# Performance work log

Measured on AMD Instinct MI355X. Metric: run time of the kernel, lower is better.

The kernel has to match this reference:

```python
import jax, jax.numpy as jnp
import numpy as np


def _quantize(mat):
    # per-row (last-dim) symmetric int8 quantization; scale stored in fp16 like torch
    max_val = (jnp.max(jnp.abs(mat), axis=-1) / 127.0).astype(jnp.float16)
    # torch's .to(int8) truncates toward zero; jnp astype does the same for in-range values
    q = (mat / max_val[..., None].astype(mat.dtype)).astype(jnp.int8)
    return q, max_val


def setup_inputs() -> dict:
    key = jax.random.key(0)
    k1, k2, k3, k4 = jax.random.split(key, 4)
    B, S, D_IN, D_OUT = 4, 2048, 4096, 4096
    x = jax.random.normal(k1, (B, S, D_IN), dtype=jnp.float32)
    origin_weight = jax.random.normal(k2, (D_OUT, D_IN), dtype=jnp.float32) * 0.02
    bias = jax.random.normal(k3, (D_OUT,), dtype=jnp.float32) * 0.01
    act_max = jax.random.normal(k4, (D_IN,), dtype=jnp.float32)
    return {"x": x, "origin_weight": origin_weight, "bias": bias,
            "act_max": act_max, "alpha": 32}


def reference(x, origin_weight, bias, act_max, alpha):
    d_in = act_max.shape[-1]
    # get_unq_idx_topk: top-alpha outlier channels by |act_max|
    _, idx = jax.lax.top_k(jnp.abs(act_max), alpha)          # [alpha]
    t = jnp.ones((d_in,), dtype=origin_weight.dtype).at[idx].set(0)

    # weight decomposition + quantization (done in __init__ in torch)
    weight_q, w_max = _quantize(origin_weight * t)           # [out,in] int8, [out] fp16
    weight_unq = origin_weight[:, idx].T                      # [alpha, out]

    # activation decomposition + per-token quantization
    x_unq = x[..., idx]                                       # [B,S,alpha]
    x_q, x_max = _quantize(x * t.astype(x.dtype))             # [B,S,in] int8, [B,S] fp16

    # simulated MatMulInteger: int8 values multiplied in fp32
    res_q = jnp.matmul(x_q.astype(jnp.float32), weight_q.T.astype(jnp.float32))  # [B,S,out]
    mx = (x_max[..., None] * w_max[None, :]).astype(jnp.float32)                  # [B,S,out]
    res_q = (res_q * mx).astype(x.dtype)

    # fp outlier path
    res_unq = jnp.matmul(x_unq, weight_unq) + bias
    return res_q + res_unq
```

## Files before the change

kernel.cpp:

```cpp
#include <hip/hip_runtime.h>
#include <hip/hip_fp16.h>

typedef __attribute__((ext_vector_type(4)))  int   i32x4;
typedef __attribute__((ext_vector_type(16))) int   i32x16;

#define ALPHA 32
#define BM 256
#define BN 128
#define BK 64


__global__ __launch_bounds__(256) void topk_kernel(const float* __restrict__ act_max,
                                                   int* __restrict__ idx_out,
                                                   unsigned* __restrict__ tbits,
                                                   int K) {
  __shared__ float v[4096];
  __shared__ float rv[4];
  __shared__ int   ri[4];
  __shared__ unsigned bits[128];
  const int t = threadIdx.x;
  for (int i = t; i < K; i += 256) v[i] = fabsf(act_max[i]);
  for (int i = t; i < K / 32; i += 256) bits[i] = 0xFFFFFFFFu;
  __syncthreads();
  for (int sel = 0; sel < ALPHA; ++sel) {
    float bv = -1.f; int bi = 0;
    for (int i = t; i < K; i += 256) {
      float x = v[i];
      if (x > bv) { bv = x; bi = i; }
    }
    for (int m = 1; m < 64; m <<= 1) {
      float ov = __shfl_xor(bv, m);
      int   oi = __shfl_xor(bi, m);
      if (ov > bv || (ov == bv && oi < bi)) { bv = ov; bi = oi; }
    }
    if ((t & 63) == 0) { rv[t >> 6] = bv; ri[t >> 6] = bi; }
    __syncthreads();
    if (t == 0) {
      for (int u = 1; u < 4; ++u)
        if (rv[u] > bv || (rv[u] == bv && ri[u] < bi)) { bv = rv[u]; bi = ri[u]; }
      idx_out[sel] = bi;
      v[bi] = -2.f;
      bits[bi >> 5] &= ~(1u << (bi & 31));
    }
    __syncthreads();
  }
  for (int i = t; i < K / 32; i += 256) tbits[i] = bits[i];
}

__global__ __launch_bounds__(256) void quant8_kernel(
    const float* __restrict__ srcW, const float* __restrict__ srcX,
    const unsigned* __restrict__ tbits, const int* __restrict__ idxg,
    signed char* __restrict__ wq, signed char* __restrict__ xq,
    _Float16* __restrict__ wmax, _Float16* __restrict__ xmax,
    float* __restrict__ wuf, float* __restrict__ xuf,
    int nbw, int K, int N, int M) {
  const int t = threadIdx.x, lane = t & 63, w = t >> 6;
  const int b = blockIdx.x;
  const float* src; signed char* q; _Float16* smax; float* unq; int r0, R;
  if (b < nbw) { src = srcW; q = wq; smax = wmax; unq = wuf; r0 = b * 8; R = N; }
  else         { src = srcX; q = xq; smax = xmax; unq = xuf; r0 = (b - nbw) * 8; R = M; }
  __shared__ unsigned bits[128];
  __shared__ signed char qt[8 * 4096];
  for (int i = t; i < 128; i += 256) bits[i] = tbits[i];
  __syncthreads();
  const int shft = (lane & 7) * 4;
#pragma unroll
  for (int g = 0; g < 2; ++g) {
    const int rl = w + 4 * g;
    const float4* srow = (const float4*)(src + (size_t)(r0 + rl) * K);
    float4 v[16];
    float am = 0.f;
#pragma unroll
    for (int j = 0; j < 16; ++j) {
      float4 x = srow[j * 64 + lane];
      unsigned b4 = bits[j * 8 + (lane >> 3)] >> shft;
      if (!(b4 & 1u)) x.x = 0.f;
      if (!(b4 & 2u)) x.y = 0.f;
      if (!(b4 & 4u)) x.z = 0.f;
      if (!(b4 & 8u)) x.w = 0.f;
      v[j] = x;
      am = fmaxf(am, fmaxf(fmaxf(fabsf(x.x), fabsf(x.y)), fmaxf(fabsf(x.z), fabsf(x.w))));
    }
#pragma unroll
    for (int m = 1; m < 64; m <<= 1) am = fmaxf(am, __shfl_xor(am, m));
    const _Float16 sh = (_Float16)(am / 127.0f);
    const float s = (float)sh;
    if (lane == 0) smax[r0 + rl] = sh;
    signed char* row = qt + rl * 4096;
#pragma unroll
    for (int j = 0; j < 16; ++j) {
      float4 x = v[j];
      char4 c;
      c.x = (signed char)(x.x / s);
      c.y = (signed char)(x.y / s);
      c.z = (signed char)(x.z / s);
      c.w = (signed char)(x.w / s);
      const int c2 = j * 16 + (lane >> 2);
      *(char4*)(row + ((c2 ^ rl) << 4) + (lane & 3) * 4) = c;
    }
  }
  __syncthreads();
  const size_t pbase = (size_t)(r0 >> 5) * 32 * K + (size_t)(r0 & 31) * 16;
#pragma unroll
  for (int i = 0; i < 8; ++i) {
    const int s2 = i * 256 + t;
    const int c2 = s2 >> 3, rl = s2 & 7;
    int4 d = *(const int4*)(qt + rl * 4096 + ((c2 ^ rl) << 4));
    *(int4*)(q + pbase + (size_t)c2 * 512 + rl * 16) = d;
  }
  {
    const int j = t >> 3, rl = t & 7;
    unq[(size_t)j * R + r0 + rl] = src[(size_t)(r0 + rl) * K + idxg[j]];
  }
}

__device__ __forceinline__ void gld_lds16(const signed char* g, signed char* l) {
  __builtin_amdgcn_global_load_lds(
      (const __attribute__((address_space(1))) void*)g,
      (__attribute__((address_space(3))) void*)l, 16, 0, 0);
}

__global__ __launch_bounds__(256, 2) void gemm_kernel(
    const signed char* __restrict__ xq, const signed char* __restrict__ wq,
    const _Float16* __restrict__ xmax, const _Float16* __restrict__ wmax,
    const float* __restrict__ xuf,
    const float* __restrict__ wuf,
    const float* __restrict__ bias,
    float* __restrict__ out, int M, int N, int K) {
  __shared__ union {
    signed char A[4][BM * BK];
    struct { float xu[ALPHA * BM]; float wu[ALPHA * BN]; } e;
  } sm;
  __shared__ _Float16 xmh[BM];
  __shared__ _Float16 wmh[BN];
  __shared__ float    bl[BN];

  const int t = threadIdx.x;
  const int bid = blockIdx.y * gridDim.x + blockIdx.x;
  const int xcd = bid & 7, loc = bid >> 3;
  const int bxi = xcd * 4 + (loc & 3);
  const int byi = loc >> 2;
  const int bm0 = byi * BM;
  const int bn0 = bxi * BN;
  const int lane = t & 63, w = t >> 6;
  const int wm = w >> 1, wn = w & 1;
  const int hi = lane >> 5, l31 = lane & 31;

  i32x16 acc[4][2] = {};

  const size_t P32 = (size_t)32 * K;
  const signed char* aS = xq + (size_t)bm0 * K + (size_t)(t >> 7) * P32 + (t & 127) * 16;
  signed char* const aD = &sm.A[0][0] + t * 16;
  const signed char* bW = wq + (size_t)(bn0 + wn * 64) * K + hi * 512 + l31 * 16;

#define STAGE_A(BUF, KT)                                                          \
  {                                                                               \
    const size_t ko = (size_t)(KT) * 2048;                                        \
    _Pragma("unroll") for (int i = 0; i < 4; ++i)                                 \
      gld_lds16(aS + (size_t)(2 * i) * P32 + ko, aD + (BUF) * (BM * BK) + i * 4096); \
  }

#define LOADB(DST, KT)                                                            \
  _Pragma("unroll") for (int ni = 0; ni < 2; ++ni)                                \
    _Pragma("unroll") for (int ks = 0; ks < 2; ++ks)                              \
      DST[ni][ks] = *(const i32x4*)(bW + (size_t)ni * 32 * K +                    \
                                    (size_t)(KT) * 2048 + ks * 1024);

#define ITER(KT, BCUR, BNXT, WCNT, DOB, DOST)                                     \
  {                                                                               \
    asm volatile("s_waitcnt vmcnt(" #WCNT ")" ::: "memory");                      \
    asm volatile("s_barrier" ::: "memory");                                       \
    if (DOB) { LOADB(BNXT, (KT) + 1); }                                           \
    if (DOST) { STAGE_A(((KT) + 2) & 3, (KT) + 2); }                              \
    const signed char* aRd = &sm.A[(KT) & 3][0] + (wm * 4) * 2048 + hi * 512 + l31 * 16; \
    i32x4 af[2][4];                                                               \
    _Pragma("unroll") for (int ks = 0; ks < 2; ++ks)                              \
      _Pragma("unroll") for (int mi = 0; mi < 4; ++mi)                            \
        af[ks][mi] = *(const i32x4*)(aRd + mi * 2048 + ks * 1024);                \
    __builtin_amdgcn_s_setprio(1);                                                \
    _Pragma("unroll") for (int ks = 0; ks < 2; ++ks)                              \
      _Pragma("unroll") for (int ni = 0; ni < 2; ++ni)                            \
        _Pragma("unroll") for (int mi = 0; mi < 4; ++mi)                          \
          acc[mi][ni] = __builtin_amdgcn_mfma_i32_32x32x32_i8(                    \
              af[ks][mi], BCUR[ni][ks], acc[mi][ni], 0, 0, 0);                    \
    __builtin_amdgcn_s_setprio(0);                                                \
  }

  const int NT = K >> 6;
  i32x4 bA[2][2], bB[2][2];
  STAGE_A(0, 0);
  STAGE_A(1, 1);
  LOADB(bA, 0);

  int kt = 0;
  for (; kt < NT - 2; kt += 2) {
    ITER(kt,     bA, bB, 8, true, true);
    ITER(kt + 1, bB, bA, 8, true, (kt + 3 < NT));
  }
  ITER(NT - 2, bA, bB, 8, true,  false);
  ITER(NT - 1, bB, bA, 4, false, false);
#undef ITER
#undef LOADB
#undef STAGE_A

  __syncthreads();
  {
    const float4* xs = (const float4*)xuf;
    float4* xl = (float4*)sm.e.xu;
#pragma unroll
    for (int i = 0; i < 8; ++i) {
      int p = i * 256 + t;
      int j = p >> 6, r4 = p & 63;
      xl[p] = xs[(size_t)j * (M >> 2) + (bm0 >> 2) + r4];
    }
    const float4* wsrc = (const float4*)wuf;
    float4* wl = (float4*)sm.e.wu;
#pragma unroll
    for (int i = 0; i < 4; ++i) {
      int p = i * 256 + t;
      int j = p >> 5, r4 = p & 31;
      wl[p] = wsrc[(size_t)j * (N >> 2) + (bn0 >> 2) + r4];
    }
    if (t < BM / 2) ((unsigned*)xmh)[t] = ((const unsigned*)(xmax + bm0))[t];
    if (t < BN / 2) ((unsigned*)wmh)[t] = ((const unsigned*)(wmax + bn0))[t];
    if (t < BN / 4) ((float4*)bl)[t] = ((const float4*)(bias + bn0))[t];
  }
  __syncthreads();

  const int c0 = wn * 64 + l31;
  const _Float16 wh0 = wmh[c0], wh1 = wmh[c0 + 32];
  const float bv0 = bl[c0], bv1 = bl[c0 + 32];
  const float* xul = sm.e.xu;
  const float* wul = sm.e.wu;

#pragma unroll
  for (int mi = 0; mi < 4; ++mi) {
    const int rbase = wm * 128 + mi * 32 + 4 * hi;
    float f0[16], f1[16];
#pragma unroll
    for (int r = 0; r < 16; ++r) {
      int row = rbase + (r & 3) + 8 * (r >> 2);
      _Float16 xh = xmh[row];
      float mx0 = (float)(_Float16)(xh * wh0);
      float mx1 = (float)(_Float16)(xh * wh1);
      f0[r] = (float)acc[mi][0][r] * mx0 + bv0;
      f1[r] = (float)acc[mi][1][r] * mx1 + bv1;
    }
#pragma unroll 4
    for (int j = 0; j < ALPHA; ++j) {
      const float4* xrow4 = (const float4*)(xul + j * BM + rbase);
      float wv0 = wul[j * BN + c0];
      float wv1 = wul[j * BN + c0 + 32];
#pragma unroll
      for (int gq = 0; gq < 4; ++gq) {
        float4 xv = xrow4[gq * 2];
        f0[gq * 4 + 0] += xv.x * wv0;  f1[gq * 4 + 0] += xv.x * wv1;
        f0[gq * 4 + 1] += xv.y * wv0;  f1[gq * 4 + 1] += xv.y * wv1;
        f0[gq * 4 + 2] += xv.z * wv0;  f1[gq * 4 + 2] += xv.z * wv1;
        f0[gq * 4 + 3] += xv.w * wv0;  f1[gq * 4 + 3] += xv.w * wv1;
      }
    }
#pragma unroll
    for (int r = 0; r < 16; ++r) {
      int row = bm0 + rbase + (r & 3) + 8 * (r >> 2);
      size_t o = (size_t)row * N + bn0;
      out[o + c0] = f0[r];
      out[o + c0 + 32] = f1[r];
    }
  }
}

extern "C" void kernel_launch(void* const* d_in, const int* in_sizes, int n_in,
                              void* d_out, int out_size, void* d_ws, size_t ws_size,
                              hipStream_t stream) {
  const float* x       = (const float*)d_in[0];
  const float* W       = (const float*)d_in[1];
  const float* bias    = (const float*)d_in[2];
  const float* act_max = (const float*)d_in[3];
  const int K = in_sizes[3];
  const int N = in_sizes[1] / K;
  const int M = in_sizes[0] / K;
  float* out = (float*)d_out;

  char* ws = (char*)d_ws;
  size_t off = 0;
  auto take = [&](size_t b) { char* p = ws + off; off += (b + 255) & ~(size_t)255; return p; };
  signed char* wq  = (signed char*)take((size_t)N * K);
  signed char* xq  = (signed char*)take((size_t)M * K);
  _Float16* wmax   = (_Float16*)take((size_t)N * 2);
  _Float16* xmax   = (_Float16*)take((size_t)M * 2);
  float* wuf       = (float*)take((size_t)ALPHA * N * 4);
  float* xuf       = (float*)take((size_t)ALPHA * M * 4);
  int* idx         = (int*)take(ALPHA * 4);
  unsigned* tbits  = (unsigned*)take((size_t)(K / 32) * 4);

  const int nbw = N / 8, nbx = M / 8;
  topk_kernel<<<1, 256, 0, stream>>>(act_max, idx, tbits, K);
  quant8_kernel<<<nbw + nbx, 256, 0, stream>>>(W, x, tbits, idx, wq, xq,
                                               wmax, xmax, wuf, xuf, nbw, K, N, M);
  dim3 grid(N / BN, M / BM);
  gemm_kernel<<<grid, 256, 0, stream>>>(xq, wq, xmax, wmax, xuf, wuf, bias, out, M, N, K);
}
```

Before: 288.9 us.

## Load A and B MFMA fragments directly from global into registers, drop LDS staging

Removes the LDS staging of the A tile (global_load_lds with a 4-buffer ring and per-iteration barriers). Each wave now loads both its A and B fragments straight from global memory into registers, using double-buffered register fragments, and no barriers remain in the main loop. This cuts LDS traffic and synchronisation. In exchange, A tiles are no longer shared between the two waves in a row of the block, so global/L2 read traffic for A doubles and register pressure rises.

After: 291.9 us. No clear change (+1.1%).

```diff
diff --git a/kernel.cpp b/kernel.cpp
--- a/kernel.cpp
+++ b/kernel.cpp
@@ -114,11 +114,7 @@
   }
 }
 
-__device__ __forceinline__ void gld_lds16(const signed char* g, signed char* l) {
-  __builtin_amdgcn_global_load_lds(
-      (const __attribute__((address_space(1))) void*)g,
-      (__attribute__((address_space(3))) void*)l, 16, 0, 0);
-}
+typedef struct { i32x4 a[4][2]; i32x4 b[2][2]; } Frag;
 
 __global__ __launch_bounds__(256, 2) void gemm_kernel(
     const signed char* __restrict__ xq, const signed char* __restrict__ wq,
@@ -127,10 +123,7 @@
     const float* __restrict__ wuf,
     const float* __restrict__ bias,
     float* __restrict__ out, int M, int N, int K) {
-  __shared__ union {
-    signed char A[4][BM * BK];
-    struct { float xu[ALPHA * BM]; float wu[ALPHA * BN]; } e;
-  } sm;
+  __shared__ struct { float xu[ALPHA * BM]; float wu[ALPHA * BN]; } sme;
   __shared__ _Float16 xmh[BM];
   __shared__ _Float16 wmh[BN];
   __shared__ float    bl[BN];
@@ -149,64 +142,51 @@
   i32x16 acc[4][2] = {};
 
   const size_t P32 = (size_t)32 * K;
-  const signed char* aS = xq + (size_t)bm0 * K + (size_t)(t >> 7) * P32 + (t & 127) * 16;
-  signed char* const aD = &sm.A[0][0] + t * 16;
-  const signed char* bW = wq + (size_t)(bn0 + wn * 64) * K + hi * 512 + l31 * 16;
-
-#define STAGE_A(BUF, KT)                                                          \
+  const signed char* const aF = xq + ((size_t)(bm0 >> 5) + wm * 4) * P32 + hi * 512 + l31 * 16;
+  const signed char* const bF = wq + ((size_t)(bn0 >> 5) + wn * 2) * P32 + hi * 512 + l31 * 16;
+
+#define LOADT(P, KT)                                                              \
   {                                                                               \
     const size_t ko = (size_t)(KT) * 2048;                                        \
-    _Pragma("unroll") for (int i = 0; i < 4; ++i)                                 \
-      gld_lds16(aS + (size_t)(2 * i) * P32 + ko, aD + (BUF) * (BM * BK) + i * 4096); \
-  }
-
-#define LOADB(DST, KT)                                                            \
-  _Pragma("unroll") for (int ni = 0; ni < 2; ++ni)                                \
-    _Pragma("unroll") for (int ks = 0; ks < 2; ++ks)                              \
-      DST[ni][ks] = *(const i32x4*)(bW + (size_t)ni * 32 * K +                    \
-                                    (size_t)(KT) * 2048 + ks * 1024);
-
-#define ITER(KT, BCUR, BNXT, WCNT, DOB, DOST)                                     \
+    _Pragma("unroll") for (int mi = 0; mi < 4; ++mi)                              \
+      _Pragma("unroll") for (int ks = 0; ks < 2; ++ks)                            \
+        P.a[mi][ks] = *(const i32x4*)(aF + (size_t)mi * P32 + ko + ks * 1024);    \
+    _Pragma("unroll") for (int ni = 0; ni < 2; ++ni)                              \
+      _Pragma("unroll") for (int ks = 0; ks < 2; ++ks)                            \
+        P.b[ni][ks] = *(const i32x4*)(bF + (size_t)ni * P32 + ko + ks * 1024);    \
+  }
+
+#define MFMAT(P)                                                                  \
   {                                                                               \
-    asm volatile("s_waitcnt vmcnt(" #WCNT ")" ::: "memory");                      \
-    asm volatile("s_barrier" ::: "memory");                                       \
-    if (DOB) { LOADB(BNXT, (KT) + 1); }                                           \
-    if (DOST) { STAGE_A(((KT) + 2) & 3, (KT) + 2); }                              \
-    const signed char* aRd = &sm.A[(KT) & 3][0] + (wm * 4) * 2048 + hi * 512 + l31 * 16; \
-    i32x4 af[2][4];                                                               \
+    __builtin_amdgcn_s_setprio(1);                                                \
     _Pragma("unroll") for (int ks = 0; ks < 2; ++ks)                              \
       _Pragma("unroll") for (int mi = 0; mi < 4; ++mi)                            \
-        af[ks][mi] = *(const i32x4*)(aRd + mi * 2048 + ks * 1024);                \
-    __builtin_amdgcn_s_setprio(1);                                                \
-    _Pragma("unroll") for (int ks = 0; ks < 2; ++ks)                              \
-      _Pragma("unroll") for (int ni = 0; ni < 2; ++ni)                            \
-        _Pragma("unroll") for (int mi = 0; mi < 4; ++mi)                          \
+        _Pragma("unroll") for (int ni = 0; ni < 2; ++ni)                          \
           acc[mi][ni] = __builtin_amdgcn_mfma_i32_32x32x32_i8(                    \
-              af[ks][mi], BCUR[ni][ks], acc[mi][ni], 0, 0, 0);                    \
+              P.a[mi][ks], P.b[ni][ks], acc[mi][ni], 0, 0, 0);                    \
     __builtin_amdgcn_s_setprio(0);                                                \
   }
 
   const int NT = K >> 6;
-  i32x4 bA[2][2], bB[2][2];
-  STAGE_A(0, 0);
-  STAGE_A(1, 1);
-  LOADB(bA, 0);
-
+  Frag pA, pB;
+  LOADT(pA, 0);
   int kt = 0;
   for (; kt < NT - 2; kt += 2) {
-    ITER(kt,     bA, bB, 8, true, true);
-    ITER(kt + 1, bB, bA, 8, true, (kt + 3 < NT));
-  }
-  ITER(NT - 2, bA, bB, 8, true,  false);
-  ITER(NT - 1, bB, bA, 4, false, false);
-#undef ITER
-#undef LOADB
-#undef STAGE_A
+    LOADT(pB, kt + 1);
+    MFMAT(pA);
+    LOADT(pA, kt + 2);
+    MFMAT(pB);
+  }
+  LOADT(pB, NT - 1);
+  MFMAT(pA);
+  MFMAT(pB);
+#undef LOADT
+#undef MFMAT
 
   __syncthreads();
   {
     const float4* xs = (const float4*)xuf;
-    float4* xl = (float4*)sm.e.xu;
+    float4* xl = (float4*)sme.xu;
 #pragma unroll
     for (int i = 0; i < 8; ++i) {
       int p = i * 256 + t;
@@ -214,7 +194,7 @@
       xl[p] = xs[(size_t)j * (M >> 2) + (bm0 >> 2) + r4];
     }
     const float4* wsrc = (const float4*)wuf;
-    float4* wl = (float4*)sm.e.wu;
+    float4* wl = (float4*)sme.wu;
 #pragma unroll
     for (int i = 0; i < 4; ++i) {
       int p = i * 256 + t;
@@ -230,8 +210,8 @@
   const int c0 = wn * 64 + l31;
   const _Float16 wh0 = wmh[c0], wh1 = wmh[c0 + 32];
   const float bv0 = bl[c0], bv1 = bl[c0 + 32];
-  const float* xul = sm.e.xu;
-  const float* wul = sm.e.wu;
+  const float* xul = sme.xu;
+  const float* wul = sme.wu;
 
 #pragma unroll
   for (int mi = 0; mi < 4; ++mi) {
```

## Stage weight tiles through LDS with triple-buffered A/B and register-prefetched A fragments

Applied to the files above, without the earlier changes.

Replaces the four-deep A-only LDS ring plus direct global loads of B into registers with a three-deep ring that stages both A and B tiles into LDS via global_load_lds. A fragments for the next k-step are prefetched from LDS into registers during the current step, and B fragments are read from LDS each step. This aims to share weight loads across waves and overlap LDS reads with MFMA work. The trade-off is a full vmcnt(0) wait each iteration, dropped setprio hints, and higher register pressure. The quantize kernel also moves its outlier-column gather ahead of the barrier.

After: 289.4 us. No clear change (+0.2%).

```diff
diff --git a/kernel.cpp b/kernel.cpp
--- a/kernel.cpp
+++ b/kernel.cpp
@@ -99,6 +99,10 @@
       *(char4*)(row + ((c2 ^ rl) << 4) + (lane & 3) * 4) = c;
     }
   }
+  {
+    const int j = t >> 3, rl = t & 7;
+    unq[(size_t)j * R + r0 + rl] = src[(size_t)(r0 + rl) * K + idxg[j]];
+  }
   __syncthreads();
   const size_t pbase = (size_t)(r0 >> 5) * 32 * K + (size_t)(r0 & 31) * 16;
 #pragma unroll
@@ -107,10 +111,6 @@
     const int c2 = s2 >> 3, rl = s2 & 7;
     int4 d = *(const int4*)(qt + rl * 4096 + ((c2 ^ rl) << 4));
     *(int4*)(q + pbase + (size_t)c2 * 512 + rl * 16) = d;
-  }
-  {
-    const int j = t >> 3, rl = t & 7;
-    unq[(size_t)j * R + r0 + rl] = src[(size_t)(r0 + rl) * K + idxg[j]];
   }
 }
 
@@ -128,7 +128,7 @@
     const float* __restrict__ bias,
     float* __restrict__ out, int M, int N, int K) {
   __shared__ union {
-    signed char A[4][BM * BK];
+    struct { signed char A[3][BM * BK]; signed char B[3][BN * BK]; } g;
     struct { float xu[ALPHA * BM]; float wu[ALPHA * BN]; } e;
   } sm;
   __shared__ _Float16 xmh[BM];
@@ -150,58 +150,66 @@
 
   const size_t P32 = (size_t)32 * K;
   const signed char* aS = xq + (size_t)bm0 * K + (size_t)(t >> 7) * P32 + (t & 127) * 16;
-  signed char* const aD = &sm.A[0][0] + t * 16;
-  const signed char* bW = wq + (size_t)(bn0 + wn * 64) * K + hi * 512 + l31 * 16;
-
-#define STAGE_A(BUF, KT)                                                          \
+  const signed char* bS = wq + (size_t)bn0 * K + (size_t)(t >> 7) * P32 + (t & 127) * 16;
+  signed char* const aD = &sm.g.A[0][0] + t * 16;
+  signed char* const bD = &sm.g.B[0][0] + t * 16;
+  const signed char* const aR0 = &sm.g.A[0][0] + (wm * 4) * 2048 + 16 * lane;
+  const signed char* const bR0 = &sm.g.B[0][0] + (wn * 2) * 2048 + 16 * lane;
+
+#define STAGE(BUF, KT)                                                            \
   {                                                                               \
     const size_t ko = (size_t)(KT) * 2048;                                        \
     _Pragma("unroll") for (int i = 0; i < 4; ++i)                                 \
       gld_lds16(aS + (size_t)(2 * i) * P32 + ko, aD + (BUF) * (BM * BK) + i * 4096); \
-  }
-
-#define LOADB(DST, KT)                                                            \
-  _Pragma("unroll") for (int ni = 0; ni < 2; ++ni)                                \
-    _Pragma("unroll") for (int ks = 0; ks < 2; ++ks)                              \
-      DST[ni][ks] = *(const i32x4*)(bW + (size_t)ni * 32 * K +                    \
-                                    (size_t)(KT) * 2048 + ks * 1024);
-
-#define ITER(KT, BCUR, BNXT, WCNT, DOB, DOST)                                     \
+    _Pragma("unroll") for (int i = 0; i < 2; ++i)                                 \
+      gld_lds16(bS + (size_t)(2 * i) * P32 + ko, bD + (BUF) * (BN * BK) + i * 4096); \
+  }
+
+#define BODY(KT, AC, AN, CB)                                                      \
   {                                                                               \
-    asm volatile("s_waitcnt vmcnt(" #WCNT ")" ::: "memory");                      \
+    const int cb_ = (CB);                                                         \
+    const int nb_ = (cb_ + 1 == 3) ? 0 : cb_ + 1;                                 \
+    const int sb_ = (nb_ + 1 == 3) ? 0 : nb_ + 1;                                 \
+    asm volatile("s_waitcnt vmcnt(0)" ::: "memory");        \
     asm volatile("s_barrier" ::: "memory");                                       \
-    if (DOB) { LOADB(BNXT, (KT) + 1); }                                           \
-    if (DOST) { STAGE_A(((KT) + 2) & 3, (KT) + 2); }                              \
-    const signed char* aRd = &sm.A[(KT) & 3][0] + (wm * 4) * 2048 + hi * 512 + l31 * 16; \
-    i32x4 af[2][4];                                                               \
+    i32x4 bf[2][2];                                                               \
+    _Pragma("unroll") for (int ni = 0; ni < 2; ++ni)                              \
+      _Pragma("unroll") for (int ks = 0; ks < 2; ++ks)                            \
+        bf[ni][ks] = *(const i32x4*)(bR0 + cb_ * (BN * BK) + ni * 2048 + ks * 1024); \
+    if ((KT) + 2 < NT) STAGE(sb_, (KT) + 2);                                      \
+    if ((KT) + 1 < NT) {                                                          \
+      _Pragma("unroll") for (int ks = 0; ks < 2; ++ks)                            \
+        _Pragma("unroll") for (int mi = 0; mi < 4; ++mi)                          \
+          AN[ks][mi] = *(const i32x4*)(aR0 + nb_ * (BM * BK) + mi * 2048 + ks * 1024); \
+    }                                                                             \
     _Pragma("unroll") for (int ks = 0; ks < 2; ++ks)                              \
       _Pragma("unroll") for (int mi = 0; mi < 4; ++mi)                            \
-        af[ks][mi] = *(const i32x4*)(aRd + mi * 2048 + ks * 1024);                \
-    __builtin_amdgcn_s_setprio(1);                                                \
-    _Pragma("unroll") for (int ks = 0; ks < 2; ++ks)                              \
-      _Pragma("unroll") for (int ni = 0; ni < 2; ++ni)                            \
-        _Pragma("unroll") for (int mi = 0; mi < 4; ++mi)                          \
+        _Pragma("unroll") for (int ni = 0; ni < 2; ++ni)                          \
           acc[mi][ni] = __builtin_amdgcn_mfma_i32_32x32x32_i8(                    \
-              af[ks][mi], BCUR[ni][ks], acc[mi][ni], 0, 0, 0);                    \
-    __builtin_amdgcn_s_setprio(0);                                                \
+              AC[ks][mi], bf[ni][ks], acc[mi][ni], 0, 0, 0);                      \
   }
 
   const int NT = K >> 6;
-  i32x4 bA[2][2], bB[2][2];
-  STAGE_A(0, 0);
-  STAGE_A(1, 1);
-  LOADB(bA, 0);
-
-  int kt = 0;
-  for (; kt < NT - 2; kt += 2) {
-    ITER(kt,     bA, bB, 8, true, true);
-    ITER(kt + 1, bB, bA, 8, true, (kt + 3 < NT));
-  }
-  ITER(NT - 2, bA, bB, 8, true,  false);
-  ITER(NT - 1, bB, bA, 4, false, false);
-#undef ITER
-#undef LOADB
-#undef STAGE_A
+  i32x4 aX[2][4], aY[2][4];
+  STAGE(0, 0);
+  STAGE(1, 1);
+  asm volatile("s_waitcnt vmcnt(6)" ::: "memory");
+  asm volatile("s_barrier" ::: "memory");
+#pragma unroll
+  for (int ks = 0; ks < 2; ++ks)
+#pragma unroll
+    for (int mi = 0; mi < 4; ++mi)
+      aX[ks][mi] = *(const i32x4*)(aR0 + mi * 2048 + ks * 1024);
+
+  int cb = 0;
+  for (int kt = 0; kt < NT; kt += 2) {
+    const int cbB = (cb + 1 == 3) ? 0 : cb + 1;
+    BODY(kt,     aX, aY, cb);
+    BODY(kt + 1, aY, aX, cbB);
+    cb = (cb + 2) % 3;
+  }
+#undef BODY
+#undef STAGE
 
   __syncthreads();
   {
```
